# Kernel optimization log

Hardware: AMD Instinct MI355X
Metric: run time of the kernel (lower is better)

Reference implementation:

```python
import jax, jax.numpy as jnp
import numpy as np

SIZE = 4096
LOG_N = 12  # log2(SIZE)
BATCH = 8192


def setup_inputs() -> dict:
    key = jax.random.key(0)
    k1, k2 = jax.random.split(key)
    x = jax.random.normal(k1, (BATCH, SIZE), dtype=jnp.float32)
    # one (SIZE//2, 2, 2) real twiddle bank per layer, stacked; init ~ randn/sqrt(2)
    twiddles = jax.random.normal(k2, (LOG_N, SIZE // 2, 2, 2), dtype=jnp.float32) / np.sqrt(2.0).astype(np.float32)
    return {"x": x, "twiddles": twiddles}


def _butterfly_forward(x, twiddles):
    # x: [B, n]; twiddles: [log_n, n//2, 2, 2]
    B, n = x.shape
    log_n = twiddles.shape[0]
    out = x
    for layer in range(log_n):
        stride = 2 ** (log_n - layer - 1)
        n_blocks = n // (2 * stride)
        # block b, offset i: top = out[:, b, 0, i], bot = out[:, b, 1, i]
        xr = out.reshape(B, n_blocks, 2, stride)
        top = xr[:, :, 0, :]  # [B, nb, stride]
        bot = xr[:, :, 1, :]
        # twiddle_idx = b*stride + i  ->  reshape to (nb, stride, 2, 2)
        w = twiddles[layer].reshape(n_blocks, stride, 2, 2)
        new_top = w[None, :, :, 0, 0] * top + w[None, :, :, 0, 1] * bot
        new_bot = w[None, :, :, 1, 0] * top + w[None, :, :, 1, 1] * bot
        out = jnp.stack([new_top, new_bot], axis=2).reshape(B, n)
    return out


def reference(x, twiddles):
    return _butterfly_forward(x, twiddles)
```

## Files before the change

kernel.cpp:

```cpp
#include <hip/hip_runtime.h>

#define ROWS 4
#define N 4096
#define BATCH 8192
#define PAD_STRIDE 264
#define BUF_WORDS (16 * PAD_STRIDE)

typedef float v4f __attribute__((ext_vector_type(4)));

__device__ __forceinline__ void layer_compute(float (&v)[ROWS][16],
                                              const float4 (&w)[8],
                                              const int bit) {
    const int d = 1 << bit;
    #pragma unroll
    for (int pc = 0; pc < 8; ++pc) {
        const int lo = ((pc >> bit) << (bit + 1)) | (pc & (d - 1));
        const int hi = lo + d;
        #pragma unroll
        for (int r = 0; r < ROWS; ++r) {
            const float top = v[r][lo];
            const float bot = v[r][hi];
            v[r][lo] = w[pc].x * top + w[pc].y * bot;
            v[r][hi] = w[pc].z * top + w[pc].w * bot;
        }
    }
}

__global__ __launch_bounds__(256)
void permute_tw_kernel(const float* __restrict__ tw, float4* __restrict__ nws) {
    const int i = blockIdx.x * 256 + threadIdx.x;
    const int s  = i >> 11;
    const int j  = i & 2047;
    const int pc = j >> 8;
    const int a  = (j >> 4) & 15;
    const int cb = j & 15;
    const float4* tw4 = (const float4*)tw;
    const int src = (s < 4) ? (a * 128 + pc * 16 + cb)
                            : (a * 128 + cb * 8 + pc);
    nws[i] = tw4[(4 + s) * 2048 + src];
}

__global__ __launch_bounds__(256, 3)
void butterfly_kernel(const float* __restrict__ x,
                      const float* __restrict__ tw,
                      const float4* __restrict__ nws,
                      float* __restrict__ out) {
    __shared__ float lds[BUF_WORDS];
    const int t   = threadIdx.x;
    const int thi = t >> 4;
    const int tlo = t & 15;
    const int row0 = blockIdx.x * ROWS;

    const float4* tw4 = (const float4*)tw;

    float v[ROWS][16];

    #pragma unroll
    for (int r = 0; r < ROWS; ++r) {
        const float* xr = x + (size_t)(row0 + r) * N + t;
        #pragma unroll
        for (int a = 0; a < 16; ++a)
            v[r][a] = __builtin_nontemporal_load(xr + a * 256);
    }

    #pragma unroll
    for (int l = 0; l < 4; ++l) {
        float4 w[8];
        #pragma unroll
        for (int pc = 0; pc < 8; ++pc)
            w[pc] = tw4[l * 2048 + pc * 256 + t];
        layer_compute(v, w, 3 - l);
    }

    #pragma unroll
    for (int r = 0; r < ROWS; ++r) {
        #pragma unroll
        for (int a = 0; a < 16; ++a)
            lds[a * PAD_STRIDE + t] = v[r][a];
        __syncthreads();
        #pragma unroll
        for (int b = 0; b < 16; ++b)
            v[r][b] = lds[thi * PAD_STRIDE + b * 16 + tlo];
        __syncthreads();
    }

    #pragma unroll
    for (int l = 4; l < 8; ++l) {
        float4 w[8];
        #pragma unroll
        for (int pc = 0; pc < 8; ++pc)
            w[pc] = nws[(l - 4) * 2048 + pc * 256 + t];
        layer_compute(v, w, 3 - (l - 4));
    }

    #pragma unroll
    for (int r = 0; r < ROWS; ++r) {
        #pragma unroll
        for (int b = 0; b < 16; ++b)
            lds[thi * PAD_STRIDE + b * 16 + tlo] = v[r][b];
        __syncthreads();
        const float* bp = &lds[thi * PAD_STRIDE + tlo * 16];
        #pragma unroll
        for (int q = 0; q < 4; ++q) {
            v4f c4 = *(const v4f*)(bp + 4 * q);
            v[r][4 * q + 0] = c4.x;
            v[r][4 * q + 1] = c4.y;
            v[r][4 * q + 2] = c4.z;
            v[r][4 * q + 3] = c4.w;
        }
        if (r != ROWS - 1) __syncthreads();
    }

    #pragma unroll
    for (int l = 8; l < 12; ++l) {
        float4 w[8];
        #pragma unroll
        for (int pc = 0; pc < 8; ++pc)
            w[pc] = nws[(l - 4) * 2048 + pc * 256 + t];
        layer_compute(v, w, 3 - (l - 8));
    }

    v4f* lf = (v4f*)lds;
    #pragma unroll
    for (int r = 0; r < ROWS; ++r) {
        __syncthreads();
        #pragma unroll
        for (int q = 0; q < 4; ++q) {
            v4f s4;
            s4.x = v[r][4 * q + 0];
            s4.y = v[r][4 * q + 1];
            s4.z = v[r][4 * q + 2];
            s4.w = v[r][4 * q + 3];
            lf[4 * t + q] = s4;
        }
        __syncthreads();
        float* orow = out + (size_t)(row0 + r) * N;
        #pragma unroll
        for (int k = 0; k < 4; ++k) {
            v4f s4 = lf[k * 256 + t];
            __builtin_nontemporal_store(s4, (v4f*)orow + k * 256 + t);
        }
    }
}

__global__ __launch_bounds__(256, 3)
void butterfly_kernel_fb(const float* __restrict__ x,
                         const float* __restrict__ tw,
                         float* __restrict__ out) {
    __shared__ float lds[BUF_WORDS];
    const int t   = threadIdx.x;
    const int thi = t >> 4;
    const int tlo = t & 15;
    const int row0 = blockIdx.x * ROWS;
    const float4* tw4 = (const float4*)tw;
    float v[ROWS][16];
    #pragma unroll
    for (int r = 0; r < ROWS; ++r) {
        const float* xr = x + (size_t)(row0 + r) * N + t;
        #pragma unroll
        for (int a = 0; a < 16; ++a)
            v[r][a] = __builtin_nontemporal_load(xr + a * 256);
    }
    #pragma unroll
    for (int l = 0; l < 4; ++l) {
        float4 w[8];
        #pragma unroll
        for (int pc = 0; pc < 8; ++pc) w[pc] = tw4[l * 2048 + pc * 256 + t];
        layer_compute(v, w, 3 - l);
    }
    #pragma unroll
    for (int r = 0; r < ROWS; ++r) {
        #pragma unroll
        for (int a = 0; a < 16; ++a) lds[a * PAD_STRIDE + t] = v[r][a];
        __syncthreads();
        #pragma unroll
        for (int b = 0; b < 16; ++b) v[r][b] = lds[thi * PAD_STRIDE + b * 16 + tlo];
        __syncthreads();
    }
    #pragma unroll
    for (int l = 4; l < 8; ++l) {
        float4 w[8];
        #pragma unroll
        for (int pc = 0; pc < 8; ++pc) w[pc] = tw4[l * 2048 + thi * 128 + pc * 16 + tlo];
        layer_compute(v, w, 3 - (l - 4));
    }
    #pragma unroll
    for (int r = 0; r < ROWS; ++r) {
        #pragma unroll
        for (int b = 0; b < 16; ++b) lds[thi * PAD_STRIDE + b * 16 + tlo] = v[r][b];
        __syncthreads();
        const float* bp = &lds[thi * PAD_STRIDE + tlo * 16];
        #pragma unroll
        for (int q = 0; q < 4; ++q) {
            v4f c4 = *(const v4f*)(bp + 4 * q);
            v[r][4 * q + 0] = c4.x; v[r][4 * q + 1] = c4.y;
            v[r][4 * q + 2] = c4.z; v[r][4 * q + 3] = c4.w;
        }
        if (r != ROWS - 1) __syncthreads();
    }
    #pragma unroll
    for (int l = 8; l < 12; ++l) {
        float4 w[8];
        #pragma unroll
        for (int pc = 0; pc < 8; ++pc) w[pc] = tw4[l * 2048 + thi * 128 + tlo * 8 + pc];
        layer_compute(v, w, 3 - (l - 8));
    }
    #pragma unroll
    for (int r = 0; r < ROWS; ++r) {
        float* orow = out + (size_t)(row0 + r) * N + 16 * t;
        #pragma unroll
        for (int q = 0; q < 4; ++q) {
            v4f s4;
            s4.x = v[r][4 * q + 0]; s4.y = v[r][4 * q + 1];
            s4.z = v[r][4 * q + 2]; s4.w = v[r][4 * q + 3];
            *(v4f*)(orow + 4 * q) = s4;
        }
    }
}

extern "C" void kernel_launch(void* const* d_in, const int* in_sizes, int n_in,
                              void* d_out, int out_size, void* d_ws, size_t ws_size,
                              hipStream_t stream) {
    const float* x  = (const float*)d_in[0];
    const float* tw = (const float*)d_in[1];
    float* out      = (float*)d_out;
    dim3 block(256);
    if (ws_size >= 8u * 2048u * 16u) {
        float4* nws = (float4*)d_ws;
        hipLaunchKernelGGL(permute_tw_kernel, dim3(64), block, 0, stream, tw, nws);
        hipLaunchKernelGGL(butterfly_kernel, dim3(BATCH / ROWS), block, 0, stream,
                           x, tw, nws, out);
    } else {
        hipLaunchKernelGGL(butterfly_kernel_fb, dim3(BATCH / ROWS), block, 0, stream,
                           x, tw, out);
    }
}
```

Baseline: 77.41 us.

## Restructure butterfly into radix-8 stages with 512 threads and three LDS transposes

Replaces the radix-16 decomposition (16 values per row per thread, 256 threads, two LDS exchanges) with a radix-8 one: 512 threads each hold 8 values per row and run four 3-layer stages with three padded LDS transposes in between. A new permutation kernel reorders twiddles for layers 3–11 so every stage reads them coalesced. Halving the per-thread register footprint is meant to raise occupancy and hide memory latency, at the cost of an extra LDS round trip and more barriers. The final store now writes directly from registers with a stride-8 pattern rather than going through an LDS staging step.

```diff
diff --git a/kernel.cpp b/kernel.cpp
--- a/kernel.cpp
+++ b/kernel.cpp
@@ -1,144 +1,201 @@
 #include <hip/hip_runtime.h>
 
-#define ROWS 4
 #define N 4096
 #define BATCH 8192
+#define NROWS 4
+#define TPB 512
+#define D2S 68
+#define D3S 544
+#define ROWBUF 4352
+#define NWS_F4 (9 * 2048)
+
+typedef float v4f __attribute__((ext_vector_type(4)));
+
+__device__ __forceinline__ void bfly(float (&v)[NROWS][8], const float4 (&w)[4], const int k) {
+    const int bit = 2 - k;
+    const int d = 1 << bit;
+    #pragma unroll
+    for (int pc = 0; pc < 4; ++pc) {
+        const int lo = ((pc >> bit) << (bit + 1)) | (pc & (d - 1));
+        const int hi = lo + d;
+        #pragma unroll
+        for (int r = 0; r < NROWS; ++r) {
+            const float top = v[r][lo], bot = v[r][hi];
+            v[r][lo] = w[pc].x * top + w[pc].y * bot;
+            v[r][hi] = w[pc].z * top + w[pc].w * bot;
+        }
+    }
+}
+
+__global__ __launch_bounds__(256)
+void permute_tw8(const float* __restrict__ tw, float4* __restrict__ nws) {
+    const int i = blockIdx.x * 256 + threadIdx.x;
+    const int li = i >> 11;
+    const int j  = i & 2047;
+    const int pc = j >> 9;
+    const int t  = j & 511;
+    const int l  = 3 + li;
+    const int s  = l / 3, k = l % 3, B = 11 - l;
+    const int bit = 2 - k, d = 1 << bit;
+    const int lo = ((pc >> bit) << (bit + 1)) | (pc & (d - 1));
+    int d3, d2, d1, d0;
+    if (s == 1)      { d3 = t >> 6; d1 = (t >> 3) & 7; d0 = t & 7; d2 = lo; }
+    else if (s == 2) { d3 = t >> 6; d2 = (t >> 3) & 7; d0 = t & 7; d1 = lo; }
+    else             { d3 = t >> 6; d2 = (t >> 3) & 7; d1 = t & 7; d0 = lo; }
+    const int e = (d3 << 9) | (d2 << 6) | (d1 << 3) | d0;
+    const int src = ((e >> (B + 1)) << B) | (e & ((1 << B) - 1));
+    nws[i] = ((const float4*)tw)[l * 2048 + src];
+}
+
+__global__ __launch_bounds__(512, 4)
+void bfly8_kernel(const float* __restrict__ x,
+                  const float* __restrict__ tw,
+                  const float4* __restrict__ nws,
+                  float* __restrict__ out) {
+    __shared__ float lds[2 * ROWBUF];
+    const int t = threadIdx.x;
+    const int row0 = blockIdx.x * NROWS;
+    const float4* tw4 = (const float4*)tw;
+
+    float v[NROWS][8];
+
+    #pragma unroll
+    for (int r = 0; r < NROWS; ++r) {
+        const float* xr = x + (size_t)(row0 + r) * N + t;
+        #pragma unroll
+        for (int d3 = 0; d3 < 8; ++d3)
+            v[r][d3] = __builtin_nontemporal_load(xr + d3 * 512);
+    }
+
+    #pragma unroll
+    for (int k = 0; k < 3; ++k) {
+        float4 w[4];
+        #pragma unroll
+        for (int pc = 0; pc < 4; ++pc)
+            w[pc] = tw4[k * 2048 + pc * 512 + t];
+        bfly(v, w, k);
+    }
+
+    #pragma unroll
+    for (int h = 0; h < 2; ++h) {
+        #pragma unroll
+        for (int rr = 0; rr < 2; ++rr) {
+            float* buf = lds + rr * ROWBUF;
+            const int base = ((t >> 6) * D2S) + (t & 63);
+            #pragma unroll
+            for (int d3 = 0; d3 < 8; ++d3)
+                buf[d3 * D3S + base] = v[2 * h + rr][d3];
+        }
+        __syncthreads();
+        #pragma unroll
+        for (int rr = 0; rr < 2; ++rr) {
+            const float* buf = lds + rr * ROWBUF;
+            const int base = ((t >> 6) * D3S) + (t & 63);
+            #pragma unroll
+            for (int d2 = 0; d2 < 8; ++d2)
+                v[2 * h + rr][d2] = buf[base + d2 * D2S];
+        }
+        __syncthreads();
+    }
+
+    #pragma unroll
+    for (int k = 0; k < 3; ++k) {
+        float4 w[4];
+        #pragma unroll
+        for (int pc = 0; pc < 4; ++pc)
+            w[pc] = nws[(k) * 2048 + pc * 512 + t];
+        bfly(v, w, k);
+    }
+
+    #pragma unroll
+    for (int h = 0; h < 2; ++h) {
+        #pragma unroll
+        for (int rr = 0; rr < 2; ++rr) {
+            float* buf = lds + rr * ROWBUF;
+            const int base = ((t >> 6) * D3S) + (t & 63);
+            #pragma unroll
+            for (int d2 = 0; d2 < 8; ++d2)
+                buf[base + d2 * D2S] = v[2 * h + rr][d2];
+        }
+        __syncthreads();
+        #pragma unroll
+        for (int rr = 0; rr < 2; ++rr) {
+            const float* buf = lds + rr * ROWBUF;
+            const int base = ((t >> 6) * D3S) + (((t >> 3) & 7) * D2S) + (t & 7);
+            #pragma unroll
+            for (int d1 = 0; d1 < 8; ++d1)
+                v[2 * h + rr][d1] = buf[base + d1 * 8];
+        }
+        __syncthreads();
+    }
+
+    #pragma unroll
+    for (int k = 0; k < 3; ++k) {
+        float4 w[4];
+        #pragma unroll
+        for (int pc = 0; pc < 4; ++pc)
+            w[pc] = nws[(3 + k) * 2048 + pc * 512 + t];
+        bfly(v, w, k);
+    }
+
+    #pragma unroll
+    for (int h = 0; h < 2; ++h) {
+        #pragma unroll
+        for (int rr = 0; rr < 2; ++rr) {
+            float* buf = lds + rr * ROWBUF;
+            const int base = ((t >> 6) * D3S) + (((t >> 3) & 7) * D2S) + (t & 7);
+            #pragma unroll
+            for (int d1 = 0; d1 < 8; ++d1)
+                buf[base + d1 * 8] = v[2 * h + rr][d1];
+        }
+        __syncthreads();
+        #pragma unroll
+        for (int rr = 0; rr < 2; ++rr) {
+            const float* buf = lds + rr * ROWBUF;
+            const int base = ((t >> 6) * D3S) + (((t >> 3) & 7) * D2S) + ((t & 7) * 8);
+            v4f lo4 = *(const v4f*)(buf + base);
+            v4f hi4 = *(const v4f*)(buf + base + 4);
+            float (&vr)[8] = v[2 * h + rr];
+            vr[0] = lo4.x; vr[1] = lo4.y; vr[2] = lo4.z; vr[3] = lo4.w;
+            vr[4] = hi4.x; vr[5] = hi4.y; vr[6] = hi4.z; vr[7] = hi4.w;
+        }
+        if (h == 0) __syncthreads();
+    }
+
+    #pragma unroll
+    for (int k = 0; k < 3; ++k) {
+        float4 w[4];
+        #pragma unroll
+        for (int pc = 0; pc < 4; ++pc)
+            w[pc] = nws[(6 + k) * 2048 + pc * 512 + t];
+        bfly(v, w, k);
+    }
+
+    #pragma unroll
+    for (int r = 0; r < NROWS; ++r) {
+        float* orow = out + (size_t)(row0 + r) * N + 8 * t;
+        v4f s0, s1;
+        s0.x = v[r][0]; s0.y = v[r][1]; s0.z = v[r][2]; s0.w = v[r][3];
+        s1.x = v[r][4]; s1.y = v[r][5]; s1.z = v[r][6]; s1.w = v[r][7];
+        *(v4f*)(orow)     = s0;
+        *(v4f*)(orow + 4) = s1;
+    }
+}
+
 #define PAD_STRIDE 264
 #define BUF_WORDS (16 * PAD_STRIDE)
 
-typedef float v4f __attribute__((ext_vector_type(4)));
-
-__device__ __forceinline__ void layer_compute(float (&v)[ROWS][16],
-                                              const float4 (&w)[8],
-                                              const int bit) {
+__device__ __forceinline__ void layer16(float (&v)[4][16], const float4 (&w)[8], const int bit) {
     const int d = 1 << bit;
     #pragma unroll
     for (int pc = 0; pc < 8; ++pc) {
         const int lo = ((pc >> bit) << (bit + 1)) | (pc & (d - 1));
         const int hi = lo + d;
         #pragma unroll
-        for (int r = 0; r < ROWS; ++r) {
-            const float top = v[r][lo];
-            const float bot = v[r][hi];
+        for (int r = 0; r < 4; ++r) {
+            const float top = v[r][lo], bot = v[r][hi];
             v[r][lo] = w[pc].x * top + w[pc].y * bot;
             v[r][hi] = w[pc].z * top + w[pc].w * bot;
-        }
-    }
-}
-
-__global__ __launch_bounds__(256)
-void permute_tw_kernel(const float* __restrict__ tw, float4* __restrict__ nws) {
-    const int i = blockIdx.x * 256 + threadIdx.x;
-    const int s  = i >> 11;
-    const int j  = i & 2047;
-    const int pc = j >> 8;
-    const int a  = (j >> 4) & 15;
-    const int cb = j & 15;
-    const float4* tw4 = (const float4*)tw;
-    const int src = (s < 4) ? (a * 128 + pc * 16 + cb)
-                            : (a * 128 + cb * 8 + pc);
-    nws[i] = tw4[(4 + s) * 2048 + src];
-}
-
-__global__ __launch_bounds__(256, 3)
-void butterfly_kernel(const float* __restrict__ x,
-                      const float* __restrict__ tw,
-                      const float4* __restrict__ nws,
-                      float* __restrict__ out) {
-    __shared__ float lds[BUF_WORDS];
-    const int t   = threadIdx.x;
-    const int thi = t >> 4;
-    const int tlo = t & 15;
-    const int row0 = blockIdx.x * ROWS;
-
-    const float4* tw4 = (const float4*)tw;
-
-    float v[ROWS][16];
-
-    #pragma unroll
-    for (int r = 0; r < ROWS; ++r) {
-        const float* xr = x + (size_t)(row0 + r) * N + t;
-        #pragma unroll
-        for (int a = 0; a < 16; ++a)
-            v[r][a] = __builtin_nontemporal_load(xr + a * 256);
-    }
-
-    #pragma unroll
-    for (int l = 0; l < 4; ++l) {
-        float4 w[8];
-        #pragma unroll
-        for (int pc = 0; pc < 8; ++pc)
-            w[pc] = tw4[l * 2048 + pc * 256 + t];
-        layer_compute(v, w, 3 - l);
-    }
-
-    #pragma unroll
-    for (int r = 0; r < ROWS; ++r) {
-        #pragma unroll
-        for (int a = 0; a < 16; ++a)
-            lds[a * PAD_STRIDE + t] = v[r][a];
-        __syncthreads();
-        #pragma unroll
-        for (int b = 0; b < 16; ++b)
-            v[r][b] = lds[thi * PAD_STRIDE + b * 16 + tlo];
-        __syncthreads();
-    }
-
-    #pragma unroll
-    for (int l = 4; l < 8; ++l) {
-        float4 w[8];
-        #pragma unroll
-        for (int pc = 0; pc < 8; ++pc)
-            w[pc] = nws[(l - 4) * 2048 + pc * 256 + t];
-        layer_compute(v, w, 3 - (l - 4));
-    }
-
-    #pragma unroll
-    for (int r = 0; r < ROWS; ++r) {
-        #pragma unroll
-        for (int b = 0; b < 16; ++b)
-            lds[thi * PAD_STRIDE + b * 16 + tlo] = v[r][b];
-        __syncthreads();
-        const float* bp = &lds[thi * PAD_STRIDE + tlo * 16];
-        #pragma unroll
-        for (int q = 0; q < 4; ++q) {
-            v4f c4 = *(const v4f*)(bp + 4 * q);
-            v[r][4 * q + 0] = c4.x;
-            v[r][4 * q + 1] = c4.y;
-            v[r][4 * q + 2] = c4.z;
-            v[r][4 * q + 3] = c4.w;
-        }
-        if (r != ROWS - 1) __syncthreads();
-    }
-
-    #pragma unroll
-    for (int l = 8; l < 12; ++l) {
-        float4 w[8];
-        #pragma unroll
-        for (int pc = 0; pc < 8; ++pc)
-            w[pc] = nws[(l - 4) * 2048 + pc * 256 + t];
-        layer_compute(v, w, 3 - (l - 8));
-    }
-
-    v4f* lf = (v4f*)lds;
-    #pragma unroll
-    for (int r = 0; r < ROWS; ++r) {
-        __syncthreads();
-        #pragma unroll
-        for (int q = 0; q < 4; ++q) {
-            v4f s4;
-            s4.x = v[r][4 * q + 0];
-            s4.y = v[r][4 * q + 1];
-            s4.z = v[r][4 * q + 2];
-            s4.w = v[r][4 * q + 3];
-            lf[4 * t + q] = s4;
-        }
-        __syncthreads();
-        float* orow = out + (size_t)(row0 + r) * N;
-        #pragma unroll
-        for (int k = 0; k < 4; ++k) {
-            v4f s4 = lf[k * 256 + t];
-            __builtin_nontemporal_store(s4, (v4f*)orow + k * 256 + t);
         }
     }
 }
@@ -148,28 +205,26 @@
                          const float* __restrict__ tw,
                          float* __restrict__ out) {
     __shared__ float lds[BUF_WORDS];
-    const int t   = threadIdx.x;
-    const int thi = t >> 4;
-    const int tlo = t & 15;
-    const int row0 = blockIdx.x * ROWS;
+    const int t = threadIdx.x;
+    const int thi = t >> 4, tlo = t & 15;
+    const int row0 = blockIdx.x * 4;
     const float4* tw4 = (const float4*)tw;
-    float v[ROWS][16];
-    #pragma unroll
-    for (int r = 0; r < ROWS; ++r) {
+    float v[4][16];
+    #pragma unroll
+    for (int r = 0; r < 4; ++r) {
         const float* xr = x + (size_t)(row0 + r) * N + t;
         #pragma unroll
-        for (int a = 0; a < 16; ++a)
-            v[r][a] = __builtin_nontemporal_load(xr + a * 256);
+        for (int a = 0; a < 16; ++a) v[r][a] = __builtin_nontemporal_load(xr + a * 256);
     }
     #pragma unroll
     for (int l = 0; l < 4; ++l) {
         float4 w[8];
         #pragma unroll
         for (int pc = 0; pc < 8; ++pc) w[pc] = tw4[l * 2048 + pc * 256 + t];
-        layer_compute(v, w, 3 - l);
-    }
-    #pragma unroll
-    for (int r = 0; r < ROWS; ++r) {
+        layer16(v, w, 3 - l);
+    }
+    #pragma unroll
+    for (int r = 0; r < 4; ++r) {
         #pragma unroll
         for (int a = 0; a < 16; ++a) lds[a * PAD_STRIDE + t] = v[r][a];
         __syncthreads();
@@ -182,10 +237,10 @@
         float4 w[8];
         #pragma unroll
         for (int pc = 0; pc < 8; ++pc) w[pc] = tw4[l * 2048 + thi * 128 + pc * 16 + tlo];
-        layer_compute(v, w, 3 - (l - 4));
-    }
-    #pragma unroll
-    for (int r = 0; r < ROWS; ++r) {
+        layer16(v, w, 3 - (l - 4));
+    }
+    #pragma unroll
+    for (int r = 0; r < 4; ++r) {
         #pragma unroll
         for (int b = 0; b < 16; ++b) lds[thi * PAD_STRIDE + b * 16 + tlo] = v[r][b];
         __syncthreads();
@@ -196,17 +251,17 @@
             v[r][4 * q + 0] = c4.x; v[r][4 * q + 1] = c4.y;
             v[r][4 * q + 2] = c4.z; v[r][4 * q + 3] = c4.w;
         }
-        if (r != ROWS - 1) __syncthreads();
+        if (r != 3) __syncthreads();
     }
     #pragma unroll
     for (int l = 8; l < 12; ++l) {
         float4 w[8];
         #pragma unroll
         for (int pc = 0; pc < 8; ++pc) w[pc] = tw4[l * 2048 + thi * 128 + tlo * 8 + pc];
-        layer_compute(v, w, 3 - (l - 8));
-    }
-    #pragma unroll
-    for (int r = 0; r < ROWS; ++r) {
+        layer16(v, w, 3 - (l - 8));
+    }
+    #pragma unroll
+    for (int r = 0; r < 4; ++r) {
         float* orow = out + (size_t)(row0 + r) * N + 16 * t;
         #pragma unroll
         for (int q = 0; q < 4; ++q) {
@@ -224,14 +279,13 @@
     const float* x  = (const float*)d_in[0];
     const float* tw = (const float*)d_in[1];
     float* out      = (float*)d_out;
-    dim3 block(256);
-    if (ws_size >= 8u * 2048u * 16u) {
+    if (ws_size >= (size_t)NWS_F4 * 16u) {
         float4* nws = (float4*)d_ws;
-        hipLaunchKernelGGL(permute_tw_kernel, dim3(64), block, 0, stream, tw, nws);
-        hipLaunchKernelGGL(butterfly_kernel, dim3(BATCH / ROWS), block, 0, stream,
+        hipLaunchKernelGGL(permute_tw8, dim3(NWS_F4 * 16 / 4096), dim3(256), 0, stream, tw, nws);
+        hipLaunchKernelGGL(bfly8_kernel, dim3(BATCH / NROWS), dim3(TPB), 0, stream,
                            x, tw, nws, out);
     } else {
-        hipLaunchKernelGGL(butterfly_kernel_fb, dim3(BATCH / ROWS), block, 0, stream,
+        hipLaunchKernelGGL(butterfly_kernel_fb, dim3(BATCH / 4), dim3(256), 0, stream,
                            x, tw, out);
     }
 }
```

After: 86.04 us. 11.1% more time.

## Double-buffer LDS transposes two rows at a time and prefetch twiddles across barriers

Applied to the files above, without the earlier changes.

The main kernel's LDS transposes now use two buffers, so two rows are exchanged per barrier instead of one, roughly halving the number of __syncthreads. The first twiddle bank of each stage is loaded before the barrier to hide its latency. Padding is changed (stride 20 per 16-float group, and a padded v4f layout on output) to reduce bank conflicts. LDS use roughly doubles and the launch bound drops from 3 to 2 blocks per SIMD group, which lowers occupancy.

```diff
diff --git a/kernel.cpp b/kernel.cpp
--- a/kernel.cpp
+++ b/kernel.cpp
@@ -3,8 +3,10 @@
 #define ROWS 4
 #define N 4096
 #define BATCH 8192
-#define PAD_STRIDE 264
-#define BUF_WORDS (16 * PAD_STRIDE)
+#define S_AB 264
+#define HALF 5248
+#define S_BC 328
+#define NWS_F4 (8 * 2048)
 
 typedef float v4f __attribute__((ext_vector_type(4)));
 
@@ -40,12 +42,14 @@
     nws[i] = tw4[(4 + s) * 2048 + src];
 }
 
-__global__ __launch_bounds__(256, 3)
+__global__ __launch_bounds__(256, 2)
 void butterfly_kernel(const float* __restrict__ x,
                       const float* __restrict__ tw,
                       const float4* __restrict__ nws,
                       float* __restrict__ out) {
-    __shared__ float lds[BUF_WORDS];
+    __shared__ float lds[2 * HALF];
+    float* bufA = lds;
+    float* bufB = lds + HALF;
     const int t   = threadIdx.x;
     const int thi = t >> 4;
     const int tlo = t & 15;
@@ -72,20 +76,35 @@
         layer_compute(v, w, 3 - l);
     }
 
-    #pragma unroll
-    for (int r = 0; r < ROWS; ++r) {
-        #pragma unroll
-        for (int a = 0; a < 16; ++a)
-            lds[a * PAD_STRIDE + t] = v[r][a];
-        __syncthreads();
-        #pragma unroll
-        for (int b = 0; b < 16; ++b)
-            v[r][b] = lds[thi * PAD_STRIDE + b * 16 + tlo];
-        __syncthreads();
-    }
-
-    #pragma unroll
-    for (int l = 4; l < 8; ++l) {
+    float4 wB[8];
+    {
+        #pragma unroll
+        for (int a = 0; a < 16; ++a) bufA[a * S_AB + t] = v[0][a];
+        #pragma unroll
+        for (int a = 0; a < 16; ++a) bufB[a * S_AB + t] = v[1][a];
+        #pragma unroll
+        for (int pc = 0; pc < 8; ++pc)
+            wB[pc] = nws[pc * 256 + t];
+        __syncthreads();
+        #pragma unroll
+        for (int b = 0; b < 16; ++b) v[0][b] = bufA[thi * S_AB + b * 16 + tlo];
+        #pragma unroll
+        for (int b = 0; b < 16; ++b) v[1][b] = bufB[thi * S_AB + b * 16 + tlo];
+        __syncthreads();
+        #pragma unroll
+        for (int a = 0; a < 16; ++a) bufA[a * S_AB + t] = v[2][a];
+        #pragma unroll
+        for (int a = 0; a < 16; ++a) bufB[a * S_AB + t] = v[3][a];
+        __syncthreads();
+        #pragma unroll
+        for (int b = 0; b < 16; ++b) v[2][b] = bufA[thi * S_AB + b * 16 + tlo];
+        #pragma unroll
+        for (int b = 0; b < 16; ++b) v[3][b] = bufB[thi * S_AB + b * 16 + tlo];
+    }
+
+    layer_compute(v, wB, 3);
+    #pragma unroll
+    for (int l = 5; l < 8; ++l) {
         float4 w[8];
         #pragma unroll
         for (int pc = 0; pc < 8; ++pc)
@@ -93,26 +112,48 @@
         layer_compute(v, w, 3 - (l - 4));
     }
 
-    #pragma unroll
-    for (int r = 0; r < ROWS; ++r) {
-        #pragma unroll
-        for (int b = 0; b < 16; ++b)
-            lds[thi * PAD_STRIDE + b * 16 + tlo] = v[r][b];
-        __syncthreads();
-        const float* bp = &lds[thi * PAD_STRIDE + tlo * 16];
-        #pragma unroll
-        for (int q = 0; q < 4; ++q) {
-            v4f c4 = *(const v4f*)(bp + 4 * q);
-            v[r][4 * q + 0] = c4.x;
-            v[r][4 * q + 1] = c4.y;
-            v[r][4 * q + 2] = c4.z;
-            v[r][4 * q + 3] = c4.w;
-        }
-        if (r != ROWS - 1) __syncthreads();
-    }
-
-    #pragma unroll
-    for (int l = 8; l < 12; ++l) {
+    float4 wC[8];
+    {
+        __syncthreads();
+        #pragma unroll
+        for (int b = 0; b < 16; ++b) bufA[thi * S_BC + b * 20 + tlo] = v[0][b];
+        #pragma unroll
+        for (int b = 0; b < 16; ++b) bufB[thi * S_BC + b * 20 + tlo] = v[1][b];
+        #pragma unroll
+        for (int pc = 0; pc < 8; ++pc)
+            wC[pc] = nws[4 * 2048 + pc * 256 + t];
+        __syncthreads();
+        #pragma unroll
+        for (int rr = 0; rr < 2; ++rr) {
+            const float* bp = (rr ? bufB : bufA) + thi * S_BC + tlo * 20;
+            #pragma unroll
+            for (int q = 0; q < 4; ++q) {
+                v4f c4 = *(const v4f*)(bp + 4 * q);
+                v[rr][4 * q + 0] = c4.x; v[rr][4 * q + 1] = c4.y;
+                v[rr][4 * q + 2] = c4.z; v[rr][4 * q + 3] = c4.w;
+            }
+        }
+        __syncthreads();
+        #pragma unroll
+        for (int b = 0; b < 16; ++b) bufA[thi * S_BC + b * 20 + tlo] = v[2][b];
+        #pragma unroll
+        for (int b = 0; b < 16; ++b) bufB[thi * S_BC + b * 20 + tlo] = v[3][b];
+        __syncthreads();
+        #pragma unroll
+        for (int rr = 2; rr < 4; ++rr) {
+            const float* bp = (rr == 3 ? bufB : bufA) + thi * S_BC + tlo * 20;
+            #pragma unroll
+            for (int q = 0; q < 4; ++q) {
+                v4f c4 = *(const v4f*)(bp + 4 * q);
+                v[rr][4 * q + 0] = c4.x; v[rr][4 * q + 1] = c4.y;
+                v[rr][4 * q + 2] = c4.z; v[rr][4 * q + 3] = c4.w;
+            }
+        }
+    }
+
+    layer_compute(v, wC, 3);
+    #pragma unroll
+    for (int l = 9; l < 12; ++l) {
         float4 w[8];
         #pragma unroll
         for (int pc = 0; pc < 8; ++pc)
@@ -120,46 +161,60 @@
         layer_compute(v, w, 3 - (l - 8));
     }
 
-    v4f* lf = (v4f*)lds;
-    #pragma unroll
-    for (int r = 0; r < ROWS; ++r) {
-        __syncthreads();
-        #pragma unroll
-        for (int q = 0; q < 4; ++q) {
-            v4f s4;
-            s4.x = v[r][4 * q + 0];
-            s4.y = v[r][4 * q + 1];
-            s4.z = v[r][4 * q + 2];
-            s4.w = v[r][4 * q + 3];
-            lf[4 * t + q] = s4;
-        }
-        __syncthreads();
-        float* orow = out + (size_t)(row0 + r) * N;
-        #pragma unroll
-        for (int k = 0; k < 4; ++k) {
-            v4f s4 = lf[k * 256 + t];
-            __builtin_nontemporal_store(s4, (v4f*)orow + k * 256 + t);
-        }
-    }
-}
+    {
+        v4f* fA = (v4f*)bufA;
+        v4f* fB = (v4f*)bufB;
+        __syncthreads();
+        #pragma unroll
+        for (int h = 0; h < 2; ++h) {
+            #pragma unroll
+            for (int rr = 0; rr < 2; ++rr) {
+                v4f* f = rr ? fB : fA;
+                const int r = 2 * h + rr;
+                #pragma unroll
+                for (int q = 0; q < 4; ++q) {
+                    v4f s4;
+                    s4.x = v[r][4 * q + 0]; s4.y = v[r][4 * q + 1];
+                    s4.z = v[r][4 * q + 2]; s4.w = v[r][4 * q + 3];
+                    f[5 * t + q] = s4;
+                }
+            }
+            __syncthreads();
+            #pragma unroll
+            for (int rr = 0; rr < 2; ++rr) {
+                v4f* f = rr ? fB : fA;
+                const int r = 2 * h + rr;
+                float* orow = out + (size_t)(row0 + r) * N;
+                #pragma unroll
+                for (int k = 0; k < 4; ++k) {
+                    const int m = k * 256 + t;
+                    v4f s4 = f[m + (m >> 2)];
+                    __builtin_nontemporal_store(s4, (v4f*)orow + m);
+                }
+            }
+            if (h == 0) __syncthreads();
+        }
+    }
+}
+
+#define PAD_STRIDE 264
+#define BUF_WORDS (16 * PAD_STRIDE)
 
 __global__ __launch_bounds__(256, 3)
 void butterfly_kernel_fb(const float* __restrict__ x,
                          const float* __restrict__ tw,
                          float* __restrict__ out) {
     __shared__ float lds[BUF_WORDS];
-    const int t   = threadIdx.x;
-    const int thi = t >> 4;
-    const int tlo = t & 15;
-    const int row0 = blockIdx.x * ROWS;
+    const int t = threadIdx.x;
+    const int thi = t >> 4, tlo = t & 15;
+    const int row0 = blockIdx.x * 4;
     const float4* tw4 = (const float4*)tw;
-    float v[ROWS][16];
-    #pragma unroll
-    for (int r = 0; r < ROWS; ++r) {
+    float v[4][16];
+    #pragma unroll
+    for (int r = 0; r < 4; ++r) {
         const float* xr = x + (size_t)(row0 + r) * N + t;
         #pragma unroll
-        for (int a = 0; a < 16; ++a)
-            v[r][a] = __builtin_nontemporal_load(xr + a * 256);
+        for (int a = 0; a < 16; ++a) v[r][a] = __builtin_nontemporal_load(xr + a * 256);
     }
     #pragma unroll
     for (int l = 0; l < 4; ++l) {
@@ -169,7 +224,7 @@
         layer_compute(v, w, 3 - l);
     }
     #pragma unroll
-    for (int r = 0; r < ROWS; ++r) {
+    for (int r = 0; r < 4; ++r) {
         #pragma unroll
         for (int a = 0; a < 16; ++a) lds[a * PAD_STRIDE + t] = v[r][a];
         __syncthreads();
@@ -185,7 +240,7 @@
         layer_compute(v, w, 3 - (l - 4));
     }
     #pragma unroll
-    for (int r = 0; r < ROWS; ++r) {
+    for (int r = 0; r < 4; ++r) {
         #pragma unroll
         for (int b = 0; b < 16; ++b) lds[thi * PAD_STRIDE + b * 16 + tlo] = v[r][b];
         __syncthreads();
@@ -196,7 +251,7 @@
             v[r][4 * q + 0] = c4.x; v[r][4 * q + 1] = c4.y;
             v[r][4 * q + 2] = c4.z; v[r][4 * q + 3] = c4.w;
         }
-        if (r != ROWS - 1) __syncthreads();
+        if (r != 3) __syncthreads();
     }
     #pragma unroll
     for (int l = 8; l < 12; ++l) {
@@ -206,7 +261,7 @@
         layer_compute(v, w, 3 - (l - 8));
     }
     #pragma unroll
-    for (int r = 0; r < ROWS; ++r) {
+    for (int r = 0; r < 4; ++r) {
         float* orow = out + (size_t)(row0 + r) * N + 16 * t;
         #pragma unroll
         for (int q = 0; q < 4; ++q) {
@@ -225,13 +280,13 @@
     const float* tw = (const float*)d_in[1];
     float* out      = (float*)d_out;
     dim3 block(256);
-    if (ws_size >= 8u * 2048u * 16u) {
+    if (ws_size >= (size_t)NWS_F4 * 16u) {
         float4* nws = (float4*)d_ws;
         hipLaunchKernelGGL(permute_tw_kernel, dim3(64), block, 0, stream, tw, nws);
         hipLaunchKernelGGL(butterfly_kernel, dim3(BATCH / ROWS), block, 0, stream,
                            x, tw, nws, out);
     } else {
-        hipLaunchKernelGGL(butterfly_kernel_fb, dim3(BATCH / ROWS), block, 0, stream,
+        hipLaunchKernelGGL(butterfly_kernel_fb, dim3(BATCH / 4), block, 0, stream,
                            x, tw, out);
     }
 }
```

Result: no change. 76.73 us (-0.9%).
